# Optimization experiments

Hardware: AMD Instinct MI355X
Metric: run time of the kernel (lower is better)

## Reference

```python
import jax, jax.numpy as jnp
import numpy as np

E = 512
H = 8
D = E // H  # head_dim = 64
SCALE = D ** -0.5
NEG_INF = float('-inf')


def layer_norm(x, g, b, eps=1e-5):
    mu = jnp.mean(x, axis=-1, keepdims=True)
    var = jnp.var(x, axis=-1, keepdims=True)
    return (x - mu) * jax.lax.rsqrt(var + eps) * g + b


def setup_inputs() -> dict:
    key = jax.random.key(0)
    ks = jax.random.split(key, 16)
    B, Q, K = 4, 2048, 2048
    inp = {
        'query': jax.random.normal(ks[0], (B, Q, E), jnp.float32),
        'key_value': jax.random.normal(ks[1], (B, K, E), jnp.float32),
        'kv_mask': jax.random.randint(ks[2], (B, K), 0, 2) > 0,
        'sparse_mask': jax.random.randint(ks[3], (B, Q, K), 0, 2) > 0,
        'ln_q_g': jnp.ones((E,), jnp.float32),
        'ln_q_b': jnp.zeros((E,), jnp.float32),
        'ln_kv_g': jnp.ones((E,), jnp.float32),
        'ln_kv_b': jnp.zeros((E,), jnp.float32),
        # Linear weights stored as (in, out): y = x @ W + b
        'Wq': jax.random.normal(ks[4], (E, E), jnp.float32) * (E ** -0.5),
        'bq': jnp.zeros((E,), jnp.float32),
        'Wk': jax.random.normal(ks[5], (E, E), jnp.float32) * (E ** -0.5),
        'bk': jnp.zeros((E,), jnp.float32),
        'Wv': jax.random.normal(ks[6], (E, E), jnp.float32) * (E ** -0.5),
        'bv': jnp.zeros((E,), jnp.float32),
        'Wo': jax.random.normal(ks[7], (E, E), jnp.float32) * (E ** -0.5),
        'bo': jnp.zeros((E,), jnp.float32),
    }
    return inp


def reference(query, key_value, kv_mask, sparse_mask,
              ln_q_g, ln_q_b, ln_kv_g, ln_kv_b,
              Wq, bq, Wk, bk, Wv, bv, Wo, bo):
    B, Qn, _ = query.shape
    Kn = key_value.shape[1]
    qn = layer_norm(query, ln_q_g, ln_q_b)
    kvn = layer_norm(key_value, ln_kv_g, ln_kv_b)
    q = (qn @ Wq + bq).reshape(B, Qn, H, D)
    k = (kvn @ Wk + bk).reshape(B, Kn, H, D)
    v = (kvn @ Wv + bv).reshape(B, Kn, H, D)
    # scores: [B, H, Q, K]
    scores = jnp.einsum('bqhd,bkhd->bhqk', q, k) * SCALE
    mask = kv_mask[:, None, None, :] & sparse_mask[:, None, :, :]
    scores = jnp.where(mask, scores, NEG_INF)
    attn = jax.nn.softmax(scores, axis=-1)
    # nan_to_num(0): rows with no valid key -> all-zero weights
    valid_row = jnp.any(mask, axis=-1, keepdims=True)
    attn = jnp.where(valid_row, attn, 0.0)
    out = jnp.einsum('bhqk,bkhd->bqhd', attn, v).reshape(B, Qn, E)
    return out @ Wo + bo
```

## Files before the change

kernel.cpp:

```cpp
#include <hip/hip_runtime.h>
#include <hip/hip_bf16.h>
#include <math.h>

typedef unsigned short ushort_t;
typedef __attribute__((ext_vector_type(8))) __bf16 bf16x8;
typedef __attribute__((ext_vector_type(4))) float f32x4;
typedef __attribute__((ext_vector_type(16))) float f32x16;
typedef __attribute__((ext_vector_type(4))) unsigned int u32x4;

#define E_DIM 512
#define HEADS 8
#define HD 64
#define SEQ 2048
#define NROWS 8192
#define NEGF (-1e30f)
#define QSCALE 0.18033688011112042f

static __device__ __forceinline__ unsigned short f2b(float f) {
  unsigned int x;
  __builtin_memcpy(&x, &f, 4);
  x += 0x7fffu + ((x >> 16) & 1u);
  return (unsigned short)(x >> 16);
}

static __device__ __forceinline__ unsigned cvt_pk_bf16(float lo, float hi) {
  unsigned r;
  asm("v_cvt_pk_bf16_f32 %0, %1, %2" : "=v"(r) : "v"(lo), "v"(hi));
  return r;
}

static __device__ __forceinline__ float fexp2(float x) {
  float r;
  asm("v_exp_f32 %0, %1" : "=v"(r) : "v"(x));
  return r;
}

static __device__ __forceinline__ int swz(int row, int col) {
  return row * 64 + ((((col >> 3) ^ (row & 7)) & 7) << 3) + (col & 7);
}

static __device__ __forceinline__ void gl2lds16(const ushort_t* g, ushort_t* s) {
#if __has_builtin(__builtin_amdgcn_global_load_lds)
  __builtin_amdgcn_global_load_lds(
      (const __attribute__((address_space(1))) unsigned int*)(uintptr_t)g,
      (__attribute__((address_space(3))) unsigned int*)(uintptr_t)s,
      16, 0, 0);
#else
  int l = threadIdx.x & 63;
  *(u32x4*)(s + l * 8) = *(const u32x4*)g;
#endif
}

__launch_bounds__(256)
__global__ void prep_kernel(const float* __restrict__ Wq, const float* __restrict__ Wk,
                            const float* __restrict__ Wv, const float* __restrict__ Wo,
                            ushort_t* __restrict__ WT,
                            const int* __restrict__ kvm, const int* __restrict__ sp,
                            unsigned long long* __restrict__ bits,
                            const float* __restrict__ xq, const float* __restrict__ xkv,
                            const float* __restrict__ gq, const float* __restrict__ bq,
                            const float* __restrict__ gkv, const float* __restrict__ bkv,
                            ushort_t* __restrict__ yq, ushort_t* __restrict__ ykv) {
  int blk = blockIdx.x;
  int t = threadIdx.x;
  if (blk < 1024) {
    int z = blk >> 8, rem = blk & 255;
    const float* in = (z == 0) ? Wq : (z == 1) ? Wk : (z == 2) ? Wv : Wo;
    ushort_t* o = WT + (size_t)z * E_DIM * E_DIM;
    __shared__ float tile[32 * 33];
    int tx = t & 31, ty = t >> 5;
    int n0 = (rem & 15) * 32, k0 = (rem >> 4) * 32;
#pragma unroll
    for (int i = 0; i < 4; ++i) {
      int k = ty + i * 8;
      tile[k * 33 + tx] = in[(k0 + k) * E_DIM + n0 + tx];
    }
    __syncthreads();
#pragma unroll
    for (int i = 0; i < 4; ++i) {
      int n = ty + i * 8;
      o[(n0 + n) * E_DIM + k0 + tx] = f2b(tile[tx * 33 + n]);
    }
  } else if (blk < 3072) {
    int w = t >> 6, l = t & 63;
    int row = (blk - 1024) * 4 + w;
    int b = row >> 11;
    const int* sprow = sp + ((size_t)row << 11);
    const int* kvrow = kvm + (b << 11);
    unsigned long long* out = bits + ((size_t)row << 5);
#pragma unroll 4
    for (int it = 0; it < 32; ++it) {
      int k = it * 64 + l;
      unsigned long long m = __ballot(sprow[k] != 0 && kvrow[k] != 0);
      if (l == 0) out[it] = m;
    }
  } else {
    int idx = blk - 3072;
    int which = idx >> 11;
    const float* x = which ? xkv : xq;
    const float* g = which ? gkv : gq;
    const float* bb = which ? bkv : bq;
    ushort_t* y = which ? ykv : yq;
    int w = t >> 6, l = t & 63;
    int row = (idx & 2047) * 4 + w;
    f32x4 x0 = *(const f32x4*)&x[row * E_DIM + l * 8];
    f32x4 x1 = *(const f32x4*)&x[row * E_DIM + l * 8 + 4];
    float xf[8], s = 0.f, ss = 0.f;
#pragma unroll
    for (int j = 0; j < 8; ++j) {
      xf[j] = (j < 4) ? x0[j] : x1[j - 4];
      s += xf[j];
      ss += xf[j] * xf[j];
    }
#pragma unroll
    for (int off = 32; off > 0; off >>= 1) {
      s += __shfl_xor(s, off);
      ss += __shfl_xor(ss, off);
    }
    float mu = s * (1.f / 512.f);
    float var = fmaxf(ss * (1.f / 512.f) - mu * mu, 0.f);
    float rs = rsqrtf(var + 1e-5f);
    f32x4 g0 = *(const f32x4*)&g[l * 8];
    f32x4 g1 = *(const f32x4*)&g[l * 8 + 4];
    f32x4 b0 = *(const f32x4*)&bb[l * 8];
    f32x4 b1 = *(const f32x4*)&bb[l * 8 + 4];
#pragma unroll
    for (int j = 0; j < 8; ++j) {
      float gv = (j < 4) ? g0[j] : g1[j - 4];
      float bv = (j < 4) ? b0[j] : b1[j - 4];
      y[row * E_DIM + l * 8 + j] = f2b((xf[j] - mu) * rs * gv + bv);
    }
  }
}

template <int MODE>
static __device__ __forceinline__ void gemm_core128(ushort_t* lA, ushort_t* lB,
                                                    const ushort_t* __restrict__ A,
                                                    const ushort_t* __restrict__ WT,
                                                    const float* __restrict__ bias,
                                                    void* Cv, float scale, int m0, int n0) {
  int t = threadIdx.x, w = t >> 6, l = t & 63;
  int quad = l >> 4, l15 = l & 15;
  int wm_ = w >> 1, wn_ = w & 1;
  int csrc = ((l & 7) ^ (l >> 3)) * 8;
  int rln = l >> 3;

  f32x4 acc[4][4] = {};
  for (int kk = 0; kk < E_DIM; kk += 64) {
    __syncthreads();
#pragma unroll
    for (int i = 0; i < 4; ++i) {
      int r0 = i * 32 + w * 8;
      gl2lds16(&A[(size_t)(m0 + r0 + rln) * E_DIM + kk + csrc], &lA[r0 * 64]);
      gl2lds16(&WT[(size_t)(n0 + r0 + rln) * E_DIM + kk + csrc], &lB[r0 * 64]);
    }
    __syncthreads();
#pragma unroll
    for (int ks = 0; ks < 2; ++ks) {
      bf16x8 af[4], bf[4];
#pragma unroll
      for (int mt = 0; mt < 4; ++mt)
        af[mt] = *(const bf16x8*)&lA[swz(wm_ * 64 + mt * 16 + l15, ks * 32 + quad * 8)];
#pragma unroll
      for (int nt = 0; nt < 4; ++nt)
        bf[nt] = *(const bf16x8*)&lB[swz(wn_ * 64 + nt * 16 + l15, ks * 32 + quad * 8)];
#pragma unroll
      for (int mt = 0; mt < 4; ++mt)
#pragma unroll
        for (int nt = 0; nt < 4; ++nt)
          acc[mt][nt] = __builtin_amdgcn_mfma_f32_16x16x32_bf16(af[mt], bf[nt], acc[mt][nt], 0, 0, 0);
    }
  }

#pragma unroll
  for (int nt = 0; nt < 4; ++nt) {
    int col = n0 + wn_ * 64 + nt * 16 + l15;
    float bv = bias[col];
    if constexpr (MODE == 2) {
      int h = col >> 6, d = col & 63;
#pragma unroll
      for (int mt = 0; mt < 4; ++mt) {
        int row = m0 + wm_ * 64 + mt * 16 + quad * 4;
        int b = row >> 11, k = row & 2047;
        union { ushort_t u[4]; uint2 v; } pk;
#pragma unroll
        for (int r = 0; r < 4; ++r) pk.u[r] = f2b(acc[mt][nt][r] + bv);
        *(uint2*)&((ushort_t*)Cv)[((((size_t)(b * HEADS + h)) * HD + d) << 11) + k] = pk.v;
      }
    } else {
#pragma unroll
      for (int mt = 0; mt < 4; ++mt) {
#pragma unroll
        for (int r = 0; r < 4; ++r) {
          int rowm = m0 + wm_ * 64 + mt * 16 + quad * 4 + r;
          float val = (acc[mt][nt][r] + bv) * scale;
          if constexpr (MODE == 0)
            ((ushort_t*)Cv)[rowm * E_DIM + col] = f2b(val);
          else
            ((float*)Cv)[rowm * E_DIM + col] = val;
        }
      }
    }
  }
}

__launch_bounds__(256)
__global__ void gemm128_bf16(const ushort_t* __restrict__ A, const ushort_t* __restrict__ WT,
                             const float* __restrict__ bias, ushort_t* __restrict__ C, float scale) {
  __shared__ ushort_t lA[128 * 64];
  __shared__ ushort_t lB[128 * 64];
  gemm_core128<0>(lA, lB, A, WT, bias, C, scale, blockIdx.x * 128, blockIdx.y * 128);
}

__launch_bounds__(256)
__global__ void gemm128_f32(const ushort_t* __restrict__ A, const ushort_t* __restrict__ WT,
                            const float* __restrict__ bias, float* __restrict__ C) {
  __shared__ ushort_t lA[128 * 64];
  __shared__ ushort_t lB[128 * 64];
  gemm_core128<1>(lA, lB, A, WT, bias, C, 1.f, blockIdx.x * 128, blockIdx.y * 128);
}

__launch_bounds__(256)
__global__ void proj2_kernel(const ushort_t* __restrict__ qn, const ushort_t* __restrict__ WTq,
                             const float* __restrict__ bq, ushort_t* __restrict__ qp,
                             const ushort_t* __restrict__ kvn, const ushort_t* __restrict__ WTv,
                             const float* __restrict__ bv, ushort_t* __restrict__ Vt) {
  __shared__ ushort_t lA[128 * 64];
  __shared__ ushort_t lB[128 * 64];
  int m0 = blockIdx.x * 128, n0 = blockIdx.y * 128;
  if (blockIdx.z == 0) gemm_core128<0>(lA, lB, qn, WTq, bq, qp, QSCALE, m0, n0);
  else                 gemm_core128<2>(lA, lB, kvn, WTv, bv, Vt, 1.f, m0, n0);
}

__launch_bounds__(256)
__global__ void attn_kernel(const ushort_t* __restrict__ Qp, const ushort_t* __restrict__ Kp,
                            const ushort_t* __restrict__ Vt,
                            const unsigned long long* __restrict__ bits,
                            ushort_t* __restrict__ ctx) {
  __shared__ __align__(16) char smemb[40960];
  ushort_t* sQ = (ushort_t*)smemb;
  int t = threadIdx.x, w = t >> 6, l = t & 63;
  int qw = w & 1, ks = w >> 1;
  ushort_t* sK = (ushort_t*)(smemb + 8192 + ks * 8192);
  ushort_t* sV = (ushort_t*)(smemb + 24576 + ks * 8192);
  int l31 = l & 31, half = l >> 5;

  int flat = blockIdx.x;
  int work = (flat & 7) * 128 + (flat >> 3);
  int qblk = work & 31;
  int h = (work >> 5) & 7;
  int b = work >> 8;
  int q0 = qblk * 64;
  int bh = b * HEADS + h;
  int myq = qw * 32 + l31;
  int csrc = ((l & 7) ^ (l >> 3)) * 8;
  int rln = l >> 3;

#pragma unroll
  for (int it = 0; it < 2; ++it) {
    int r0 = w * 16 + it * 8;
    gl2lds16(&Qp[(size_t)(b * SEQ + q0 + r0 + rln) * E_DIM + h * HD + csrc], &sQ[r0 * 64]);
  }

  const unsigned long long* mrow = bits + ((size_t)(b * SEQ + q0 + myq) << 5);
  float ls0 = 0.f, ls1 = 0.f, ls2 = 0.f, ls3 = 0.f;
  f32x16 o0 = {}, o1 = {};
  bf16x8 qf[4];

  for (int t16 = 0; t16 < 16; ++t16) {
    int kt = t16 * 2 + ks;
    int k0 = kt * 64;
    unsigned long long wmask = mrow[kt];
    __syncthreads();
#pragma unroll
    for (int it = 0; it < 4; ++it) {
      int r0 = (it * 2 + qw) * 8;
      gl2lds16(&Kp[(size_t)(b * SEQ + k0 + r0 + rln) * E_DIM + h * HD + csrc], &sK[r0 * 64]);
      gl2lds16(&Vt[((size_t)bh * HD + r0 + rln) * SEQ + k0 + csrc], &sV[r0 * 64]);
    }
    __syncthreads();
    if (t16 == 0) {
#pragma unroll
      for (int ds = 0; ds < 4; ++ds)
        qf[ds] = *(const bf16x8*)&sQ[swz(myq, ds * 16 + 8 * half)];
    }

    f32x16 s0 = {}, s1 = {};
    __builtin_amdgcn_s_setprio(1);
#pragma unroll
    for (int ds = 0; ds < 4; ++ds) {
      bf16x8 kf0 = *(const bf16x8*)&sK[swz(l31, ds * 16 + 8 * half)];
      bf16x8 kf1 = *(const bf16x8*)&sK[swz(32 + l31, ds * 16 + 8 * half)];
      s0 = __builtin_amdgcn_mfma_f32_32x32x16_bf16(kf0, qf[ds], s0, 0, 0, 0);
      s1 = __builtin_amdgcn_mfma_f32_32x32x16_bf16(kf1, qf[ds], s1, 0, 0, 0);
    }
    __builtin_amdgcn_s_setprio(0);

    bf16x8 pf[4];
#pragma unroll
    for (int kt2 = 0; kt2 < 2; ++kt2) {
      const f32x16& sv = kt2 ? s1 : s0;
      unsigned h32 = ((unsigned)(wmask >> (32 * kt2))) >> (4 * half);
      unsigned wa[4], wb[4];
#pragma unroll
      for (int g = 0; g < 4; ++g) {
        unsigned gb = h32 >> (8 * g);
        float p0 = fexp2((gb & 1u)        ? sv[g * 4 + 0] : NEGF);
        float p1 = fexp2(((gb >> 1) & 1u) ? sv[g * 4 + 1] : NEGF);
        float p2 = fexp2(((gb >> 2) & 1u) ? sv[g * 4 + 2] : NEGF);
        float p3 = fexp2(((gb >> 3) & 1u) ? sv[g * 4 + 3] : NEGF);
        ls0 += p0; ls1 += p1; ls2 += p2; ls3 += p3;
        wa[g] = cvt_pk_bf16(p0, p1);
        wb[g] = cvt_pk_bf16(p2, p3);
      }
      asm("v_permlane32_swap_b32 %0, %1" : "+v"(wa[0]), "+v"(wa[1]));
      asm("v_permlane32_swap_b32 %0, %1" : "+v"(wb[0]), "+v"(wb[1]));
      asm("v_permlane32_swap_b32 %0, %1" : "+v"(wa[2]), "+v"(wa[3]));
      asm("v_permlane32_swap_b32 %0, %1" : "+v"(wb[2]), "+v"(wb[3]));
      union { unsigned u[4]; bf16x8 v; } f0, f1;
      f0.u[0] = wa[0]; f0.u[1] = wb[0]; f0.u[2] = wa[1]; f0.u[3] = wb[1];
      f1.u[0] = wa[2]; f1.u[1] = wb[2]; f1.u[2] = wa[3]; f1.u[3] = wb[3];
      pf[kt2 * 2 + 0] = f0.v;
      pf[kt2 * 2 + 1] = f1.v;
    }

    __builtin_amdgcn_s_setprio(1);
#pragma unroll
    for (int ksp = 0; ksp < 4; ++ksp) {
      bf16x8 vf0 = *(const bf16x8*)&sV[swz(l31, ksp * 16 + 8 * half)];
      bf16x8 vf1 = *(const bf16x8*)&sV[swz(32 + l31, ksp * 16 + 8 * half)];
      o0 = __builtin_amdgcn_mfma_f32_32x32x16_bf16(vf0, pf[ksp], o0, 0, 0, 0);
      o1 = __builtin_amdgcn_mfma_f32_32x32x16_bf16(vf1, pf[ksp], o1, 0, 0, 0);
    }
    __builtin_amdgcn_s_setprio(0);
  }

  float lsum = (ls0 + ls1) + (ls2 + ls3);
  lsum += __shfl_xor(lsum, 32);

  __syncthreads();
  float* mrg = (float*)(smemb + 8192);
  if (ks == 1) {
    float* e = mrg + (qw * 64 + l) * 33;
#pragma unroll
    for (int r = 0; r < 16; ++r) e[r] = o0[r];
#pragma unroll
    for (int r = 0; r < 16; ++r) e[16 + r] = o1[r];
    e[32] = lsum;
  }
  __syncthreads();
  if (ks == 0) {
    const float* e = mrg + (qw * 64 + l) * 33;
#pragma unroll
    for (int r = 0; r < 16; ++r) o0[r] += e[r];
#pragma unroll
    for (int r = 0; r < 16; ++r) o1[r] += e[16 + r];
    lsum += e[32];
    float inv = (lsum > 0.f) ? 1.f / lsum : 0.f;
    size_t base = (size_t)(b * SEQ + q0 + myq) * E_DIM + h * HD;
#pragma unroll
    for (int dt = 0; dt < 2; ++dt) {
      const f32x16& oo = dt ? o1 : o0;
#pragma unroll
      for (int g = 0; g < 4; ++g) {
        union { ushort_t u[4]; uint2 v; } ov;
#pragma unroll
        for (int r = 0; r < 4; ++r) ov.u[r] = f2b(oo[g * 4 + r] * inv);
        *(uint2*)&ctx[base + dt * 32 + g * 8 + 4 * half] = ov.v;
      }
    }
  }
}

extern "C" void kernel_launch(void* const* d_in, const int* in_sizes, int n_in,
                              void* d_out, int out_size, void* d_ws, size_t ws_size,
                              hipStream_t stream) {
  const float* query     = (const float*)d_in[0];
  const float* key_value = (const float*)d_in[1];
  const int*   kv_mask   = (const int*)d_in[2];
  const int*   sp_mask   = (const int*)d_in[3];
  const float* ln_q_g  = (const float*)d_in[4];
  const float* ln_q_b  = (const float*)d_in[5];
  const float* ln_kv_g = (const float*)d_in[6];
  const float* ln_kv_b = (const float*)d_in[7];
  const float* Wq = (const float*)d_in[8];
  const float* bq = (const float*)d_in[9];
  const float* Wk = (const float*)d_in[10];
  const float* bk = (const float*)d_in[11];
  const float* Wv = (const float*)d_in[12];
  const float* bv = (const float*)d_in[13];
  const float* Wo = (const float*)d_in[14];
  const float* bo = (const float*)d_in[15];

  const size_t NB = (size_t)NROWS * E_DIM;
  char* ws = (char*)d_ws;
  ushort_t* bufA = (ushort_t*)ws;
  ushort_t* bufB = bufA + NB;
  ushort_t* WT   = bufB + NB;
  ushort_t* WTq = WT;
  ushort_t* WTk = WTq + E_DIM * E_DIM;
  ushort_t* WTv = WTk + E_DIM * E_DIM;
  ushort_t* WTo = WTv + E_DIM * E_DIM;
  unsigned long long* bits = (unsigned long long*)(WTo + E_DIM * E_DIM);

  ushort_t* dlo = (ushort_t*)d_out;
  ushort_t* dhi = dlo + NB;

  prep_kernel<<<7168, 256, 0, stream>>>(Wq, Wk, Wv, Wo, WT, kv_mask, sp_mask, bits,
                                        query, key_value, ln_q_g, ln_q_b, ln_kv_g, ln_kv_b,
                                        dlo, bufA);

  proj2_kernel<<<dim3(64, 4, 2), 256, 0, stream>>>(dlo, WTq, bq, dhi,
                                                   bufA, WTv, bv, bufB);

  gemm128_bf16<<<dim3(64, 4), 256, 0, stream>>>(bufA, WTk, bk, dlo, 1.f);

  attn_kernel<<<1024, 256, 0, stream>>>(dhi, dlo, bufB, bits, bufA);

  gemm128_f32<<<dim3(64, 4), 256, 0, stream>>>(bufA, WTo, bo, (float*)d_out);
}
```

Before: 269.6 us.

## Fuse Q/K/V projections into one launch with 128x64 tiles and swizzled block order

Shrinks the projection GEMM tiles from 128x128 to 128x64 so each GEMM launches twice as many blocks. When the workspace is large enough, the K projection moves into a separate buffer and joins Q and V in a single 1536-block launch, removing one kernel launch and its serial dependency. Block indices are remapped in groups of eight, likely to improve L2 locality across the chiplet dies. Smaller tiles reuse each loaded A tile less and cost more global traffic per FLOP. The output GEMM uses the same smaller tile.

```diff
diff --git a/kernel.cpp b/kernel.cpp
--- a/kernel.cpp
+++ b/kernel.cpp
@@ -134,47 +134,51 @@
 }
 
 template <int MODE>
-static __device__ __forceinline__ void gemm_core128(ushort_t* lA, ushort_t* lB,
-                                                    const ushort_t* __restrict__ A,
-                                                    const ushort_t* __restrict__ WT,
-                                                    const float* __restrict__ bias,
-                                                    void* Cv, float scale, int m0, int n0) {
+static __device__ __forceinline__ void gemm_core64(ushort_t* lA, ushort_t* lB,
+                                                   const ushort_t* __restrict__ A,
+                                                   const ushort_t* __restrict__ WT,
+                                                   const float* __restrict__ bias,
+                                                   void* Cv, float scale, int m0, int n0) {
   int t = threadIdx.x, w = t >> 6, l = t & 63;
   int quad = l >> 4, l15 = l & 15;
   int wm_ = w >> 1, wn_ = w & 1;
   int csrc = ((l & 7) ^ (l >> 3)) * 8;
   int rln = l >> 3;
 
-  f32x4 acc[4][4] = {};
+  f32x4 acc[4][2] = {};
   for (int kk = 0; kk < E_DIM; kk += 64) {
     __syncthreads();
 #pragma unroll
     for (int i = 0; i < 4; ++i) {
       int r0 = i * 32 + w * 8;
       gl2lds16(&A[(size_t)(m0 + r0 + rln) * E_DIM + kk + csrc], &lA[r0 * 64]);
+    }
+#pragma unroll
+    for (int i = 0; i < 2; ++i) {
+      int r0 = i * 32 + w * 8;
       gl2lds16(&WT[(size_t)(n0 + r0 + rln) * E_DIM + kk + csrc], &lB[r0 * 64]);
     }
     __syncthreads();
 #pragma unroll
     for (int ks = 0; ks < 2; ++ks) {
-      bf16x8 af[4], bf[4];
+      bf16x8 af[4], bf[2];
 #pragma unroll
       for (int mt = 0; mt < 4; ++mt)
         af[mt] = *(const bf16x8*)&lA[swz(wm_ * 64 + mt * 16 + l15, ks * 32 + quad * 8)];
 #pragma unroll
-      for (int nt = 0; nt < 4; ++nt)
-        bf[nt] = *(const bf16x8*)&lB[swz(wn_ * 64 + nt * 16 + l15, ks * 32 + quad * 8)];
+      for (int nt = 0; nt < 2; ++nt)
+        bf[nt] = *(const bf16x8*)&lB[swz(wn_ * 32 + nt * 16 + l15, ks * 32 + quad * 8)];
 #pragma unroll
       for (int mt = 0; mt < 4; ++mt)
 #pragma unroll
-        for (int nt = 0; nt < 4; ++nt)
+        for (int nt = 0; nt < 2; ++nt)
           acc[mt][nt] = __builtin_amdgcn_mfma_f32_16x16x32_bf16(af[mt], bf[nt], acc[mt][nt], 0, 0, 0);
     }
   }
 
 #pragma unroll
-  for (int nt = 0; nt < 4; ++nt) {
-    int col = n0 + wn_ * 64 + nt * 16 + l15;
+  for (int nt = 0; nt < 2; ++nt) {
+    int col = n0 + wn_ * 32 + nt * 16 + l15;
     float bv = bias[col];
     if constexpr (MODE == 2) {
       int h = col >> 6, d = col & 63;
@@ -205,31 +209,34 @@
 }
 
 __launch_bounds__(256)
-__global__ void gemm128_bf16(const ushort_t* __restrict__ A, const ushort_t* __restrict__ WT,
-                             const float* __restrict__ bias, ushort_t* __restrict__ C, float scale) {
-  __shared__ ushort_t lA[128 * 64];
-  __shared__ ushort_t lB[128 * 64];
-  gemm_core128<0>(lA, lB, A, WT, bias, C, scale, blockIdx.x * 128, blockIdx.y * 128);
-}
-
-__launch_bounds__(256)
-__global__ void gemm128_f32(const ushort_t* __restrict__ A, const ushort_t* __restrict__ WT,
-                            const float* __restrict__ bias, float* __restrict__ C) {
-  __shared__ ushort_t lA[128 * 64];
-  __shared__ ushort_t lB[128 * 64];
-  gemm_core128<1>(lA, lB, A, WT, bias, C, 1.f, blockIdx.x * 128, blockIdx.y * 128);
-}
-
-__launch_bounds__(256)
-__global__ void proj2_kernel(const ushort_t* __restrict__ qn, const ushort_t* __restrict__ WTq,
+__global__ void proj3_kernel(const ushort_t* __restrict__ qn, const ushort_t* __restrict__ WTq,
                              const float* __restrict__ bq, ushort_t* __restrict__ qp,
                              const ushort_t* __restrict__ kvn, const ushort_t* __restrict__ WTv,
-                             const float* __restrict__ bv, ushort_t* __restrict__ Vt) {
+                             const float* __restrict__ bv, ushort_t* __restrict__ Vt,
+                             const ushort_t* __restrict__ WTk, const float* __restrict__ bk,
+                             ushort_t* __restrict__ kp, int zbase) {
   __shared__ ushort_t lA[128 * 64];
-  __shared__ ushort_t lB[128 * 64];
-  int m0 = blockIdx.x * 128, n0 = blockIdx.y * 128;
-  if (blockIdx.z == 0) gemm_core128<0>(lA, lB, qn, WTq, bq, qp, QSCALE, m0, n0);
-  else                 gemm_core128<2>(lA, lB, kvn, WTv, bv, Vt, 1.f, m0, n0);
+  __shared__ ushort_t lB[64 * 64];
+  int flat = blockIdx.x;
+  int chunk = gridDim.x >> 3;
+  int work = (flat & 7) * chunk + (flat >> 3);
+  int z = zbase + (work >> 9);
+  int r = work & 511;
+  int m0 = (r >> 3) * 128, n0 = (r & 7) * 64;
+  if (z == 0)      gemm_core64<0>(lA, lB, qn,  WTq, bq, qp, QSCALE, m0, n0);
+  else if (z == 1) gemm_core64<2>(lA, lB, kvn, WTv, bv, Vt, 1.f,    m0, n0);
+  else             gemm_core64<0>(lA, lB, kvn, WTk, bk, kp, 1.f,    m0, n0);
+}
+
+__launch_bounds__(256)
+__global__ void out_kernel(const ushort_t* __restrict__ A, const ushort_t* __restrict__ WT,
+                           const float* __restrict__ bias, float* __restrict__ C) {
+  __shared__ ushort_t lA[128 * 64];
+  __shared__ ushort_t lB[64 * 64];
+  int flat = blockIdx.x;
+  int work = (flat & 7) * 64 + (flat >> 3);
+  int m0 = (work >> 3) * 128, n0 = (work & 7) * 64;
+  gemm_core64<1>(lA, lB, A, WT, bias, C, 1.f, m0, n0);
 }
 
 __launch_bounds__(256)
@@ -402,20 +409,32 @@
   ushort_t* WTv = WTk + E_DIM * E_DIM;
   ushort_t* WTo = WTv + E_DIM * E_DIM;
   unsigned long long* bits = (unsigned long long*)(WTo + E_DIM * E_DIM);
+  ushort_t* bufC = (ushort_t*)(ws + (20u << 20));
 
   ushort_t* dlo = (ushort_t*)d_out;
   ushort_t* dhi = dlo + NB;
+
+  bool fused = ws_size >= (28u << 20);
+  ushort_t* kp = fused ? bufC : dlo;
 
   prep_kernel<<<7168, 256, 0, stream>>>(Wq, Wk, Wv, Wo, WT, kv_mask, sp_mask, bits,
                                         query, key_value, ln_q_g, ln_q_b, ln_kv_g, ln_kv_b,
                                         dlo, bufA);
 
-  proj2_kernel<<<dim3(64, 4, 2), 256, 0, stream>>>(dlo, WTq, bq, dhi,
-                                                   bufA, WTv, bv, bufB);
-
-  gemm128_bf16<<<dim3(64, 4), 256, 0, stream>>>(bufA, WTk, bk, dlo, 1.f);
-
-  attn_kernel<<<1024, 256, 0, stream>>>(dhi, dlo, bufB, bits, bufA);
-
-  gemm128_f32<<<dim3(64, 4), 256, 0, stream>>>(bufA, WTo, bo, (float*)d_out);
-}
+  if (fused) {
+    proj3_kernel<<<1536, 256, 0, stream>>>(dlo, WTq, bq, dhi,
+                                           bufA, WTv, bv, bufB,
+                                           WTk, bk, bufC, 0);
+  } else {
+    proj3_kernel<<<1024, 256, 0, stream>>>(dlo, WTq, bq, dhi,
+                                           bufA, WTv, bv, bufB,
+                                           WTk, bk, dlo, 0);
+    proj3_kernel<<<512, 256, 0, stream>>>(dlo, WTq, bq, dhi,
+                                          bufA, WTv, bv, bufB,
+                                          WTk, bk, dlo, 2);
+  }
+
+  attn_kernel<<<1024, 256, 0, stream>>>(dhi, kp, bufB, bits, bufA);
+
+  out_kernel<<<512, 256, 0, stream>>>(bufA, WTo, bo, (float*)d_out);
+}
```

Result: faster. 259.6 us (-3.7%).
